# Kernel optimization log

Measured on AMD Instinct MI355X. Metric: run time of the kernel, lower is better.

## Reference

```python
import jax, jax.numpy as jnp
import numpy as np

H = 4                      # attention heads
L_NAMES = ['self', 'cross'] * 3
K_LIST = [None, None, 128, 128, 64, 64]  # top-k per layer (None = full attention)
BN_EPS = 1e-5


def conv1d(x, W, b):
    # 1x1 Conv1d: x [B, Ci, N], W [Co, Ci], b [Co]
    return jnp.einsum('oi,bin->bon', W, x) + b[:, None]


def bn_eval(x, g, b):
    # BatchNorm1d in eval mode with running mean 0 / var 1
    inv = 1.0 / np.sqrt(1.0 + BN_EPS)
    return (g * inv)[:, None] * x + b[:, None]


def mha(x, src, Wq, bq, Wk, bk, Wv, bv, Wm, bm, k):
    B, D, N = x.shape
    dh = D // H
    q = conv1d(x, Wq, bq).reshape(B, dh, H, N)
    kk = conv1d(src, Wk, bk).reshape(B, dh, H, -1)
    v = conv1d(src, Wv, bv).reshape(B, dh, H, -1)
    scores = jnp.einsum('bdhn,bdhm->bhnm', q, kk) / np.sqrt(dh)  # [B,H,N,M]
    if k is None:
        p = jax.nn.softmax(scores, axis=-1)
        out = jnp.einsum('bhnm,bdhm->bdhn', p, v)
    else:
        vals, idx = jax.lax.top_k(scores, k)          # [B,H,N,k]
        S = jax.nn.softmax(vals, axis=-1)
        # gather value vectors at the top-k key indices: [B,dh,H,N,k]
        vg = jnp.take_along_axis(v[:, :, :, None, :], idx[:, None, :, :, :], axis=4)
        out = jnp.einsum('bhnk,bdhnk->bdhn', S, vg)
    return conv1d(out.reshape(B, D, N), Wm, bm)


def log_ot(scores, alpha, iters):
    b, m, n = scores.shape
    bins0 = jnp.broadcast_to(alpha, (b, m, 1))
    bins1 = jnp.broadcast_to(alpha, (b, 1, n))
    a = jnp.broadcast_to(alpha, (b, 1, 1))
    Z0 = jnp.concatenate([jnp.concatenate([scores, bins0], -1),
                          jnp.concatenate([bins1, a], -1)], 1)  # [b,m+1,n+1]
    norm = -np.log(float(m + n))
    log_mu = jnp.concatenate([jnp.full((m,), norm, scores.dtype),
                              jnp.array([np.log(float(n)) + norm], scores.dtype)])
    log_nu = jnp.concatenate([jnp.full((n,), norm, scores.dtype),
                              jnp.array([np.log(float(m)) + norm], scores.dtype)])
    log_mu = jnp.broadcast_to(log_mu, (b, m + 1))
    log_nu = jnp.broadcast_to(log_nu, (b, n + 1))

    def step(carry, _):
        u, v = carry
        u = log_mu - jax.nn.logsumexp(Z0 + v[:, None, :], axis=2)
        v = log_nu - jax.nn.logsumexp(Z0 + u[:, :, None], axis=1)
        return (u, v), None

    (u, v), _ = jax.lax.scan(step, (jnp.zeros_like(log_mu), jnp.zeros_like(log_nu)),
                             None, length=iters)
    return Z0 + u[:, :, None] + v[:, None, :] - norm


def _forward(desc0, desc1, Wq, bq, Wk, bk, Wv, bv, Wm, bm,
             W1, b1, g1, be1, W2, b2, Wf, bf, alpha, iters):
    d0, d1 = desc0, desc1
    for i, (name, k) in enumerate(zip(L_NAMES, K_LIST)):
        s0, s1 = (d1, d0) if name == 'cross' else (d0, d1)

        def prop(x, src):
            msg = mha(x, src, Wq[i], bq[i], Wk[i], bk[i], Wv[i], bv[i], Wm[i], bm[i], k)
            h = jnp.concatenate([x, msg], axis=1)           # [B, 2D, N]
            h = jax.nn.relu(bn_eval(conv1d(h, W1[i], b1[i]), g1[i], be1[i]))
            return conv1d(h, W2[i], b2[i])

        dlt0, dlt1 = prop(d0, s0), prop(d1, s1)
        d0, d1 = d0 + dlt0, d1 + dlt1
    m0 = conv1d(d0, Wf, bf)
    m1 = conv1d(d1, Wf, bf)
    scores = jnp.einsum('bdn,bdm->bnm', m0, m1) / np.sqrt(m0.shape[1])
    return log_ot(scores, alpha, iters)


def setup_inputs() -> dict:
    B, D, N, L = 4, 128, 1024, 6
    key = jax.random.key(0)
    ks = jax.random.split(key, 20)

    def nrm(k, shape, s):
        return jax.random.normal(k, shape, jnp.float32) * s

    sw = 1.0 / np.sqrt(D)
    return {
        'desc0': nrm(ks[0], (B, D, N), 1.0),
        'desc1': nrm(ks[1], (B, D, N), 1.0),
        'Wq': nrm(ks[2], (L, D, D), sw), 'bq': jnp.zeros((L, D), jnp.float32),
        'Wk': nrm(ks[3], (L, D, D), sw), 'bk': jnp.zeros((L, D), jnp.float32),
        'Wv': nrm(ks[4], (L, D, D), sw), 'bv': jnp.zeros((L, D), jnp.float32),
        'Wm': nrm(ks[5], (L, D, D), sw), 'bm': jnp.zeros((L, D), jnp.float32),
        'W1': nrm(ks[6], (L, 2 * D, 2 * D), 1.0 / np.sqrt(2 * D)),
        'b1': jnp.zeros((L, 2 * D), jnp.float32),
        'g1': jnp.ones((L, 2 * D), jnp.float32),
        'be1': jnp.zeros((L, 2 * D), jnp.float32),
        'W2': nrm(ks[7], (L, D, 2 * D), 1.0 / np.sqrt(2 * D)),
        'b2': jnp.zeros((L, D), jnp.float32),
        'Wf': nrm(ks[8], (D, D), sw), 'bf': jnp.zeros((D,), jnp.float32),
        'alpha': jnp.asarray(1.0, jnp.float32),
        'iters': 20,
    }


def reference(desc0, desc1, Wq, bq, Wk, bk, Wv, bv, Wm, bm,
              W1, b1, g1, be1, W2, b2, Wf, bf, alpha, iters):
    return _forward(desc0, desc1, Wq, bq, Wk, bk, Wv, bv, Wm, bm,
                    W1, b1, g1, be1, W2, b2, Wf, bf, alpha, iters)
```

## Files before the change

### kernel.cpp

```cpp
#include <hip/hip_runtime.h>
#include <hip/hip_fp16.h>
#include <stdint.h>

#define NPOS   1024
#define DMODEL 128
#define NP1    1025
#define PLP    1053700
#define PSTR   1028
#define PLPH   1057800
#define PSTRH  1032
#define NORMF  (-7.624618986159398f)
#define LOGN   (6.931471805599453f)

typedef __attribute__((ext_vector_type(8))) short s8v;
typedef __attribute__((ext_vector_type(4))) float f4v;
typedef unsigned short ushort_t;

#define MFMA(a, b, c) __builtin_amdgcn_mfma_f32_16x16x32_bf16((a), (b), (c), 0, 0, 0)

static __device__ __forceinline__ ushort_t f2bf(float f) {
    union { float f; uint32_t u; } c; c.f = f;
    uint32_t u = c.u;
    return (ushort_t)((u + 0x7fffu + ((u >> 16) & 1u)) >> 16);
}
static __device__ __forceinline__ uint32_t cvtpk(float lo, float hi) {
    uint32_t r;
    asm("v_cvt_pk_bf16_f32 %0, %1, %2" : "=v"(r) : "v"(lo), "v"(hi));
    return r;
}

#define NW0 294912
#define NW2 393216
#define NW3 196608
#define NW4 16384
#define NB5 2304
#define NPREP (NW0 + NW2 + NW3 + NW4 + NB5)
__global__ __launch_bounds__(256) void prep_weights(
    const float* __restrict__ Wq, const float* __restrict__ Wk, const float* __restrict__ Wv,
    const float* __restrict__ bq, const float* __restrict__ bk, const float* __restrict__ bv,
    const float* __restrict__ W1, const float* __restrict__ W2, const float* __restrict__ Wf,
    ushort_t* __restrict__ wqkv, ushort_t* __restrict__ w1c,
    ushort_t* __restrict__ w2, ushort_t* __restrict__ wf, float* __restrict__ bqkv)
{
    int idx = blockIdx.x * 256 + threadIdx.x;
    if (idx < NW0) {
        int l = idx / 49152, r2 = idx % 49152;
        int r = r2 / 128, i = r2 % 128;
        int sel = r >> 7, rr = r & 127;
        int o = ((rr & 31) << 2) + (rr >> 5);
        const float* src = sel == 0 ? Wq : (sel == 1 ? Wk : Wv);
        wqkv[idx] = f2bf(src[((size_t)l * 128 + o) * 128 + i]);
        return;
    }
    idx -= NW0;
    if (idx < NW2) {
        int i = idx & 255;
        if (i < 128) w1c[idx] = f2bf(W1[idx]);
        return;
    }
    idx -= NW2;
    if (idx < NW3) { w2[idx] = f2bf(W2[idx]); return; }
    idx -= NW3;
    if (idx < NW4) { wf[idx] = f2bf(Wf[idx]); return; }
    idx -= NW4;
    if (idx < NB5) {
        int l = idx / 384, r = idx % 384;
        int sel = r >> 7, rr = r & 127;
        int o = ((rr & 31) << 2) + (rr >> 5);
        const float* src = sel == 0 ? bq : (sel == 1 ? bk : bv);
        bqkv[idx] = src[l * 128 + o];
    }
}

#define NFOLD 196608
#define NFB   1536
__global__ __launch_bounds__(256) void fold_w1(
    const float* __restrict__ W1, const float* __restrict__ Wm,
    const float* __restrict__ b1, const float* __restrict__ bm,
    ushort_t* __restrict__ w1c, float* __restrict__ b1c)
{
    int idx = blockIdx.x * 256 + threadIdx.x;
    if (idx < NFOLD) {
        int l = idx / 32768, rem = idx % 32768;
        int o = rem / 128, ip = rem % 128;
        int i = ((ip & 31) << 2) + (ip >> 5);
        const float* w1row = W1 + ((size_t)l * 256 + o) * 256 + 128;
        const float* wmcol = Wm + (size_t)l * 16384 + i;
        float s = 0.f;
        #pragma unroll 8
        for (int j = 0; j < 128; ++j) s = fmaf(w1row[j], wmcol[(size_t)j * 128], s);
        w1c[((size_t)l * 256 + o) * 256 + 128 + ip] = f2bf(s);
        return;
    }
    idx -= NFOLD;
    if (idx < NFB) {
        int l = idx / 256, o = idx % 256;
        const float* w1row = W1 + ((size_t)l * 256 + o) * 256 + 128;
        const float* bml = bm + l * 128;
        float s = b1[l * 256 + o];
        #pragma unroll 8
        for (int j = 0; j < 128; ++j) s = fmaf(w1row[j], bml[j], s);
        b1c[idx] = s;
    }
}

__global__ __launch_bounds__(256) void transpose_in(
    const float* __restrict__ desc0, const float* __restrict__ desc1,
    float* __restrict__ df, ushort_t* __restrict__ db)
{
    int g = blockIdx.z;
    int nb = blockIdx.x << 6, cb = blockIdx.y << 5;
    __shared__ float sm[32][65];
    const float* S = (g < 4 ? desc0 : desc1);
    int gl = g & 3;
    {
        int row = threadIdx.x >> 3, c8 = (threadIdx.x & 7) << 3;
        const float* p = S + ((size_t)gl * 128 + cb + row) * NPOS + nb + c8;
        float4 v0 = *(const float4*)p;
        float4 v1 = *(const float4*)(p + 4);
        sm[row][c8 + 0] = v0.x; sm[row][c8 + 1] = v0.y; sm[row][c8 + 2] = v0.z; sm[row][c8 + 3] = v0.w;
        sm[row][c8 + 4] = v1.x; sm[row][c8 + 5] = v1.y; sm[row][c8 + 6] = v1.z; sm[row][c8 + 7] = v1.w;
    }
    __syncthreads();
    int n = threadIdx.x >> 2, cc = (threadIdx.x & 3) << 3;
    float y[8];
    #pragma unroll
    for (int e = 0; e < 8; ++e) y[e] = sm[cc + e][n];
    size_t base = ((size_t)g * NPOS + nb + n) * DMODEL + cb + cc;
    *(float4*)(df + base) = make_float4(y[0], y[1], y[2], y[3]);
    *(float4*)(df + base + 4) = make_float4(y[4], y[5], y[6], y[7]);
    uint4 pk = make_uint4(cvtpk(y[0], y[1]), cvtpk(y[2], y[3]),
                          cvtpk(y[4], y[5]), cvtpk(y[6], y[7]));
    *(uint4*)(db + base) = pk;
}

__global__ __launch_bounds__(256) void conv_mfma(
    const ushort_t* __restrict__ X0, int Ci,
    const ushort_t* __restrict__ W, const float* __restrict__ bias,
    ushort_t* __restrict__ outb, int Co)
{
    int g = blockIdx.z;
    int nb = blockIdx.x << 6;
    int obb = blockIdx.y << 6;
    int wave = threadIdx.x >> 6, lane = threadIdx.x & 63;
    int lrow = lane & 15, lk = (lane >> 4) << 3;
    int ob = obb + (wave << 4);
    f4v acc[4] = {};
    const ushort_t* wrow = W + (size_t)(ob + lrow) * Ci + lk;
    for (int k0 = 0; k0 < Ci; k0 += 32) {
        s8v b = *(const s8v*)(wrow + k0);
        #pragma unroll
        for (int t = 0; t < 4; ++t) {
            int n = nb + (t << 4) + lrow;
            s8v a = *(const s8v*)(X0 + ((size_t)g * NPOS + n) * Ci + k0 + lk);
            acc[t] = MFMA(a, b, acc[t]);
        }
    }
    __shared__ float sm[64][68];
    #pragma unroll
    for (int t = 0; t < 4; ++t)
        #pragma unroll
        for (int r = 0; r < 4; ++r)
            sm[(t << 4) + ((lane >> 4) << 2) + r][(wave << 4) + lrow] = acc[t][r];
    __syncthreads();
    int n = threadIdx.x >> 2, oc = (threadIdx.x & 3) << 4;
    int o0 = obb + oc;
    float y[16];
    #pragma unroll
    for (int e = 0; e < 16; ++e) y[e] = sm[n][oc + e] + bias[o0 + e];
    size_t base = ((size_t)g * NPOS + nb + n) * Co + o0;
    uint4 p0 = make_uint4(cvtpk(y[0], y[1]), cvtpk(y[2], y[3]),
                          cvtpk(y[4], y[5]), cvtpk(y[6], y[7]));
    uint4 p1 = make_uint4(cvtpk(y[8], y[9]), cvtpk(y[10], y[11]),
                          cvtpk(y[12], y[13]), cvtpk(y[14], y[15]));
    *(uint4*)(outb + base) = p0;
    *(uint4*)(outb + base + 8) = p1;
}

__global__ __launch_bounds__(256) void mlp_mfma(
    const ushort_t* __restrict__ X0, const ushort_t* __restrict__ X1,
    const ushort_t* __restrict__ W1c, const float* __restrict__ b1c,
    const float* __restrict__ bn_g, const float* __restrict__ bn_b,
    const ushort_t* __restrict__ W2w, const float* __restrict__ b2,
    float* __restrict__ resid, ushort_t* __restrict__ outb)
{
    int g = blockIdx.y;
    int nb = blockIdx.x << 4;
    __shared__ ushort_t hB[16][256];
    __shared__ float sm[16][132];
    int wave = threadIdx.x >> 6, lane = threadIdx.x & 63;
    int lrow = lane & 15, lk = (lane >> 4) << 3;
    const float BN_INV = 0.9999950000374997f;

    const ushort_t* x0p = X0 + ((size_t)g * NPOS + nb + lrow) * 128 + lk;
    const ushort_t* x1p = X1 + ((size_t)g * NPOS + nb + lrow) * 128 + lk;
    for (int p = 0; p < 4; ++p) {
        int o = (p << 6) + (wave << 4) + lrow;
        f4v acc = {};
        const ushort_t* wrow = W1c + (size_t)o * 256 + lk;
        #pragma unroll
        for (int k0 = 0; k0 < 256; k0 += 32) {
            s8v b = *(const s8v*)(wrow + k0);
            s8v a = (k0 < 128) ? *(const s8v*)(x0p + k0) : *(const s8v*)(x1p + k0 - 128);
            acc = MFMA(a, b, acc);
        }
        #pragma unroll
        for (int r = 0; r < 4; ++r)
            sm[((lane >> 4) << 2) + r][(wave << 4) + lrow] = acc[r];
        __syncthreads();
        {
            int n = threadIdx.x >> 4, oc = (threadIdx.x & 15) << 2;
            int og = (p << 6) + oc;
            float y[4];
            #pragma unroll
            for (int e = 0; e < 4; ++e) {
                float v = sm[n][oc + e] + b1c[og + e];
                y[e] = fmaxf(bn_g[og + e] * BN_INV * v + bn_b[og + e], 0.f);
            }
            *(uint2*)(&hB[n][og]) = make_uint2(cvtpk(y[0], y[1]), cvtpk(y[2], y[3]));
        }
        __syncthreads();
    }

    f4v acc2[2] = {};
    #pragma unroll
    for (int k0 = 0; k0 < 256; k0 += 32) {
        s8v a = *(const s8v*)(&hB[lrow][k0 + lk]);
        #pragma unroll
        for (int ot = 0; ot < 2; ++ot) {
            int o = (wave << 5) + (ot << 4) + lrow;
            s8v b = *(const s8v*)(W2w + (size_t)o * 256 + k0 + lk);
            acc2[ot] = MFMA(a, b, acc2[ot]);
        }
    }
    #pragma unroll
    for (int ot = 0; ot < 2; ++ot)
        #pragma unroll
        for (int r = 0; r < 4; ++r)
            sm[((lane >> 4) << 2) + r][(wave << 5) + (ot << 4) + lrow] = acc2[ot][r];
    __syncthreads();
    {
        int n = threadIdx.x >> 4, oc = (threadIdx.x & 15) << 3;
        size_t base = ((size_t)g * NPOS + nb + n) * 128 + oc;
        float* rp = resid + base;
        float4 ra = *(const float4*)rp;
        float4 rb = *(const float4*)(rp + 4);
        float y[8];
        y[0] = sm[n][oc + 0] + b2[oc + 0] + ra.x;
        y[1] = sm[n][oc + 1] + b2[oc + 1] + ra.y;
        y[2] = sm[n][oc + 2] + b2[oc + 2] + ra.z;
        y[3] = sm[n][oc + 3] + b2[oc + 3] + ra.w;
        y[4] = sm[n][oc + 4] + b2[oc + 4] + rb.x;
        y[5] = sm[n][oc + 5] + b2[oc + 5] + rb.y;
        y[6] = sm[n][oc + 6] + b2[oc + 6] + rb.z;
        y[7] = sm[n][oc + 7] + b2[oc + 7] + rb.w;
        *(float4*)rp = make_float4(y[0], y[1], y[2], y[3]);
        *(float4*)(rp + 4) = make_float4(y[4], y[5], y[6], y[7]);
        uint4 pk = make_uint4(cvtpk(y[0], y[1]), cvtpk(y[2], y[3]),
                              cvtpk(y[4], y[5]), cvtpk(y[6], y[7]));
        *(uint4*)(outb + base) = pk;
    }
}

__global__ __launch_bounds__(256) void qkv_mfma(
    const ushort_t* __restrict__ X, const ushort_t* __restrict__ W,
    const float* __restrict__ bias,
    ushort_t* __restrict__ Qb, ushort_t* __restrict__ Kb, ushort_t* __restrict__ Vb)
{
    int g = blockIdx.z;
    int nb = blockIdx.x << 6;
    int obb = blockIdx.y << 6;
    int wave = threadIdx.x >> 6, lane = threadIdx.x & 63;
    int lrow = lane & 15, lk = (lane >> 4) << 3;
    int ob = obb + (wave << 4);
    f4v acc[4] = {};
    const ushort_t* wrow = W + (size_t)(ob + lrow) * DMODEL + lk;
    for (int k0 = 0; k0 < DMODEL; k0 += 32) {
        s8v b = *(const s8v*)(wrow + k0);
        #pragma unroll
        for (int t = 0; t < 4; ++t) {
            int n = nb + (t << 4) + lrow;
            s8v a = *(const s8v*)(X + ((size_t)g * NPOS + n) * DMODEL + k0 + lk);
            acc[t] = MFMA(a, b, acc[t]);
        }
    }
    __shared__ float sm[64][68];
    #pragma unroll
    for (int t = 0; t < 4; ++t)
        #pragma unroll
        for (int r = 0; r < 4; ++r)
            sm[(t << 4) + ((lane >> 4) << 2) + r][(wave << 4) + lrow] = acc[t][r];
    __syncthreads();
    if (obb < 256) {
        int n = threadIdx.x >> 2, oc = (threadIdx.x & 3) << 4;
        int ov = obb + oc;
        ushort_t* dst = (ov < 128) ? Qb : Kb;
        int c = ov & 127;
        float y[16];
        #pragma unroll
        for (int e = 0; e < 16; ++e) y[e] = sm[n][oc + e] + bias[ov + e];
        size_t base = ((size_t)g * NPOS + nb + n) * DMODEL + c;
        uint4 p0 = make_uint4(cvtpk(y[0], y[1]), cvtpk(y[2], y[3]),
                              cvtpk(y[4], y[5]), cvtpk(y[6], y[7]));
        uint4 p1 = make_uint4(cvtpk(y[8], y[9]), cvtpk(y[10], y[11]),
                              cvtpk(y[12], y[13]), cvtpk(y[14], y[15]));
        *(uint4*)(dst + base) = p0;
        *(uint4*)(dst + base + 8) = p1;
    } else {
        int c = threadIdx.x >> 2, mc = (threadIdx.x & 3) << 4;
        float bc = bias[obb + c];
        float y[16];
        #pragma unroll
        for (int e = 0; e < 16; ++e) y[e] = sm[mc + e][c] + bc;
        size_t base = ((size_t)g * DMODEL + (obb - 256) + c) * NPOS + nb + mc;
        uint4 p0 = make_uint4(cvtpk(y[0], y[1]), cvtpk(y[2], y[3]),
                              cvtpk(y[4], y[5]), cvtpk(y[6], y[7]));
        uint4 p1 = make_uint4(cvtpk(y[8], y[9]), cvtpk(y[10], y[11]),
                              cvtpk(y[12], y[13]), cvtpk(y[14], y[15]));
        *(uint4*)(Vb + base) = p0;
        *(uint4*)(Vb + base + 8) = p1;
    }
}

__global__ __launch_bounds__(512, 8) void attn_fused(
    const ushort_t* __restrict__ Qb, const ushort_t* __restrict__ Kb,
    const ushort_t* __restrict__ Vb, ushort_t* __restrict__ ao,
    int k, int cross)
{
    __shared__ ushort_t sc[16 * 1024];
    __shared__ float sinv[16];
    int bid = blockIdx.x;
    int gh = ((bid & 7) << 2) + (bid >> 9);
    int g = gh >> 2, h = gh & 3;
    int g2 = cross ? (g ^ 4) : g;
    int n0 = ((bid >> 3) & 63) << 4;
    int wave = threadIdx.x >> 6, lane = threadIdx.x & 63;
    int lrow = lane & 15, lq = lane >> 4;

    {
        int kq = wave;
        s8v qa = *(const s8v*)(Qb + ((size_t)g * NPOS + n0 + lrow) * DMODEL
                               + (h << 5) + (lq << 3));
        const float scale = 0.17677669529663687f;
        int swz = (lrow & 7) << 4;
        const ushort_t* kb_base = Kb + ((size_t)g2 * NPOS + (kq << 7) + lrow) * DMODEL
                                  + (h << 5) + (lq << 3);
        #pragma unroll
        for (int mt = 0; mt < 8; ++mt) {
            s8v kb = *(const s8v*)(kb_base + (size_t)mt * 16 * DMODEL);
            f4v z = {};
            z = MFMA(kb, qa, z);
            uint32_t p0 = cvtpk(z[0] * scale, z[1] * scale);
            uint32_t p1 = cvtpk(z[2] * scale, z[3] * scale);
            int m = (kq << 7) + (mt << 4);
            int byte = ((lrow << 11) + ((m + (lq << 2)) << 1)) ^ swz;
            *(uint2*)((char*)sc + byte) = make_uint2(p0, p1);
        }
    }
    __syncthreads();

    {
        bool dosel = (k < NPOS);
        for (int rr = 0; rr < 2; ++rr) {
            int row = (wave << 1) + rr;
            int swz = (row & 7) << 4;
            int base = (row << 11) + (lane << 5);
            uint4 d0 = *(const uint4*)((const char*)sc + (base ^ swz));
            uint4 d1 = *(const uint4*)((const char*)sc + ((base + 16) ^ swz));
            float val[16];
            {
                uint32_t wd[8] = {d0.x, d0.y, d0.z, d0.w, d1.x, d1.y, d1.z, d1.w};
                #pragma unroll
                for (int q = 0; q < 8; ++q) {
                    union { unsigned ui; float f; } c0, c1;
                    c0.ui = wd[q] << 16; c1.ui = wd[q] & 0xFFFF0000u;
                    val[2 * q] = c0.f; val[2 * q + 1] = c1.f;
                }
            }
            float mx = val[0];
            #pragma unroll
            for (int t = 1; t < 16; ++t) mx = fmaxf(mx, val[t]);
            #pragma unroll
            for (int o = 32; o; o >>= 1) mx = fmaxf(mx, __shfl_xor(mx, o));

            unsigned selmask = 0xFFFFu;
            if (dosel) {
                unsigned prefix = 0;
                bool exact = false;
                for (int bit = 15; bit >= 0 && !exact; --bit) {
                    unsigned cand = prefix | (1u << bit);
                    unsigned craw = (cand & 0x8000u) ? (cand ^ 0x8000u) : (cand ^ 0xFFFFu);
                    union { unsigned ui; float f; } cf; cf.ui = craw << 16;
                    float cf_f = cf.f;
                    int c = 0;
                    #pragma unroll
                    for (int t = 0; t < 16; ++t)
                        c += __popcll(__ballot(val[t] >= cf_f));
                    if (c >= k) { prefix = cand; exact = (c == k); }
                }
                unsigned praw = (prefix & 0x8000u) ? (prefix ^ 0x8000u) : (prefix ^ 0xFFFFu);
                union { unsigned ui; float f; } pf; pf.ui = praw << 16;
                float thr = pf.f;
                if (exact) {
                    selmask = 0;
                    #pragma unroll
                    for (int t = 0; t < 16; ++t)
                        selmask |= (val[t] >= thr) ? (1u << t) : 0u;
                } else {
                    int cgt = 0;
                    #pragma unroll
                    for (int t = 0; t < 16; ++t)
                        cgt += __popcll(__ballot(val[t] > thr));
                    int need = k - cgt;
                    unsigned long long lmask = (1ull << lane) - 1ull;
                    int before = 0;
                    #pragma unroll
                    for (int t = 0; t < 16; ++t)
                        before += __popcll(__ballot(val[t] == thr) & lmask);
                    int loc = 0;
                    selmask = 0;
                    #pragma unroll
                    for (int t = 0; t < 16; ++t) {
                        bool tie = (val[t] == thr);
                        if ((val[t] > thr) || (tie && (before + loc < need)))
                            selmask |= (1u << t);
                        loc += tie ? 1 : 0;
                    }
                }
            }
            float sum = 0.f;
            #pragma unroll
            for (int t = 0; t < 16; ++t) {
                float wv = ((selmask >> t) & 1u) ? __expf(val[t] - mx) : 0.f;
                val[t] = wv;
                sum += wv;
            }
            #pragma unroll
            for (int o = 32; o; o >>= 1) sum += __shfl_xor(sum, o);
            if (lane == 0) sinv[row] = 1.f / sum;
            uint32_t ow[8];
            #pragma unroll
            for (int q = 0; q < 8; ++q)
                ow[q] = cvtpk(val[2 * q], val[2 * q + 1]);
            *(uint4*)((char*)sc + (base ^ swz)) = make_uint4(ow[0], ow[1], ow[2], ow[3]);
            *(uint4*)((char*)sc + ((base + 16) ^ swz)) = make_uint4(ow[4], ow[5], ow[6], ow[7]);
        }
    }
    __syncthreads();

    {
        int kquad = wave >> 1, dimg = wave & 1;
        int db = dimg << 4;
        const ushort_t* vbase = Vb + ((size_t)g2 * DMODEL + (h << 5) + db + lrow) * NPOS
                                + (kquad << 8) + (lq << 3);
        int pswz = (lrow & 7) << 4;
        int pbase = (lrow << 11) + (kquad << 9) + (lq << 4);
        f4v acc = {};
        #pragma unroll
        for (int ks = 0; ks < 8; ++ks) {
            s8v pa = *(const s8v*)((const char*)sc + ((pbase + (ks << 6)) ^ pswz));
            s8v vv = *(const s8v*)(vbase + (ks << 5));
            acc = MFMA(pa, vv, acc);
        }
        __syncthreads();
        if (kquad > 0)
            *(f4v*)((char*)sc + (((((kquad - 1) << 1) + dimg) * 64 + lane) << 4)) = acc;
        __syncthreads();
        if (kquad == 0) {
            #pragma unroll
            for (int qq = 0; qq < 3; ++qq)
                acc = acc + *(const f4v*)((char*)sc + ((((qq << 1) + dimg) * 64 + lane) << 4));
            #pragma unroll
            for (int r = 0; r < 4; ++r) {
                int rowi = (lq << 2) + r;
                int n = n0 + rowi;
                ao[((size_t)g * NPOS + n) * DMODEL + (h << 5) + db + lrow]
                    = f2bf(acc[r] * sinv[rowi]);
            }
        }
    }
}

__global__ __launch_bounds__(256) void final_mfma(
    const ushort_t* __restrict__ md, float* __restrict__ Z0P,
    __half* __restrict__ Z0H, __half* __restrict__ Z0TH)
{
    int b = blockIdx.z;
    int wave = threadIdx.x >> 6, lane = threadIdx.x & 63;
    int wr = wave >> 1, wc = wave & 1;
    int n0 = (blockIdx.y << 7) + (wr << 6);
    int m0 = (blockIdx.x << 7) + (wc << 6);
    int lrow = lane & 15, lk = (lane >> 4) << 3;
    f4v acc[4][4] = {};
    for (int k0 = 0; k0 < DMODEL; k0 += 32) {
        s8v qa[4], kb[4];
        #pragma unroll
        for (int t = 0; t < 4; ++t) {
            qa[t] = *(const s8v*)(md + ((size_t)b * NPOS + n0 + (t << 4) + lrow) * DMODEL + k0 + lk);
            kb[t] = *(const s8v*)(md + ((size_t)(b + 4) * NPOS + m0 + (t << 4) + lrow) * DMODEL + k0 + lk);
        }
        #pragma unroll
        for (int tn = 0; tn < 4; ++tn)
            #pragma unroll
            for (int tm = 0; tm < 4; ++tm)
                acc[tn][tm] = MFMA(qa[tn], kb[tm], acc[tn][tm]);
    }
    const float scf = 0.08838834764831845f;
    int rbase = (lane >> 4) << 2;
    #pragma unroll
    for (int tn = 0; tn < 4; ++tn) {
        #pragma unroll
        for (int tm = 0; tm < 4; ++tm) {
            #pragma unroll
            for (int r = 0; r < 4; ++r) {
                int n = n0 + (tn << 4) + rbase + r;
                int m = m0 + (tm << 4) + lrow;
                float y = acc[tn][tm][r] * scf;
                Z0P[(size_t)b * PLP + (size_t)n * PSTR + m] = y;
                __half hy = __float2half(y);
                Z0H [(size_t)b * PLPH + (size_t)n * PSTRH + m] = hy;
                Z0TH[(size_t)b * PLPH + (size_t)m * PSTRH + n] = hy;
            }
        }
    }
}

__global__ __launch_bounds__(1024) void ot_init(
    float* __restrict__ Z0P, __half* __restrict__ Z0H, __half* __restrict__ Z0TH,
    float* __restrict__ v, const float* __restrict__ alpha)
{
    float a = *alpha;
    __half ha = __float2half(a);
    int b = blockIdx.x, t = threadIdx.x;
    Z0P [(size_t)b * PLP  + (size_t)t * PSTR  + 1024] = a;
    Z0P [(size_t)b * PLP  + (size_t)1024 * PSTR + t] = a;
    Z0H [(size_t)b * PLPH + (size_t)t * PSTRH + 1024] = ha;
    Z0H [(size_t)b * PLPH + (size_t)1024 * PSTRH + t] = ha;
    Z0TH[(size_t)b * PLPH + (size_t)t * PSTRH + 1024] = ha;
    Z0TH[(size_t)b * PLPH + (size_t)1024 * PSTRH + t] = ha;
    v[b * NP1 + t] = 0.f;
    if (t == 0) {
        Z0P [(size_t)b * PLP  + (size_t)1024 * PSTR  + 1024] = a;
        Z0H [(size_t)b * PLPH + (size_t)1024 * PSTRH + 1024] = ha;
        Z0TH[(size_t)b * PLPH + (size_t)1024 * PSTRH + 1024] = ha;
        v[b * NP1 + 1024] = 0.f;
    }
}

__global__ __launch_bounds__(256) void lse_sweep_h(
    const __half* __restrict__ Z, const float* __restrict__ vin,
    float* __restrict__ uout)
{
    int wv = threadIdx.x >> 6, lane = threadIdx.x & 63;
    int r = blockIdx.x * 4 + wv;
    int b = r / NP1, i = r - b * NP1;
    const __half* z  = Z + (size_t)b * PLPH + (size_t)i * PSTRH;
    const float* vb = vin + b * NP1;
    float x[17];
    #pragma unroll
    for (int t = 0; t < 2; ++t) {
        int j = (t << 9) + (lane << 3);
        union { uint4 u; __half h[8]; } U;
        U.u = *(const uint4*)(z + j);
        float4 v0 = *(const float4*)(vb + j);
        float4 v1 = *(const float4*)(vb + j + 4);
        x[t * 8 + 0] = __half2float(U.h[0]) + v0.x;
        x[t * 8 + 1] = __half2float(U.h[1]) + v0.y;
        x[t * 8 + 2] = __half2float(U.h[2]) + v0.z;
        x[t * 8 + 3] = __half2float(U.h[3]) + v0.w;
        x[t * 8 + 4] = __half2float(U.h[4]) + v1.x;
        x[t * 8 + 5] = __half2float(U.h[5]) + v1.y;
        x[t * 8 + 6] = __half2float(U.h[6]) + v1.z;
        x[t * 8 + 7] = __half2float(U.h[7]) + v1.w;
    }
    x[16] = (lane == 0) ? (__half2float(z[1024]) + vb[1024]) : -1e30f;
    float m = x[0];
    #pragma unroll
    for (int t = 1; t < 17; ++t) m = fmaxf(m, x[t]);
    #pragma unroll
    for (int o = 32; o; o >>= 1) m = fmaxf(m, __shfl_xor(m, o));
    float sum = 0.f;
    #pragma unroll
    for (int t = 0; t < 17; ++t) sum += __expf(x[t] - m);
    #pragma unroll
    for (int o = 32; o; o >>= 1) sum += __shfl_xor(sum, o);
    if (lane == 0)
        uout[b * NP1 + i] = NORMF + ((i == 1024) ? LOGN : 0.f) - (m + __logf(sum));
}

__global__ __launch_bounds__(256) void ot_final(
    float* __restrict__ out, const float* __restrict__ Z0P,
    const float* __restrict__ u, const float* __restrict__ v)
{
    int r = blockIdx.x;
    int b = r / NP1, i = r - b * NP1;
    float ui = u[b * NP1 + i] - NORMF;
    const float* zp = Z0P + (size_t)b * PLP + (size_t)i * PSTR;
    float* zo = out + ((size_t)b * NP1 + i) * NP1;
    const float* vb = v + b * NP1;
    for (int j = threadIdx.x; j < NP1; j += 256) zo[j] = zp[j] + ui + vb[j];
}

extern "C" void kernel_launch(void* const* d_in, const int* in_sizes, int n_in,
                              void* d_out, int out_size, void* d_ws, size_t ws_size,
                              hipStream_t stream)
{
    (void)in_sizes; (void)n_in; (void)out_size; (void)ws_size;
    const float* desc0 = (const float*)d_in[0];
    const float* desc1 = (const float*)d_in[1];
    const float* Wq = (const float*)d_in[2];  const float* bq = (const float*)d_in[3];
    const float* Wk = (const float*)d_in[4];  const float* bk = (const float*)d_in[5];
    const float* Wv = (const float*)d_in[6];  const float* bv = (const float*)d_in[7];
    const float* Wm = (const float*)d_in[8];  const float* bm = (const float*)d_in[9];
    const float* W1 = (const float*)d_in[10]; const float* b1 = (const float*)d_in[11];
    const float* g1 = (const float*)d_in[12]; const float* be1 = (const float*)d_in[13];
    const float* W2 = (const float*)d_in[14]; const float* b2 = (const float*)d_in[15];
    const float* Wf = (const float*)d_in[16]; const float* bf = (const float*)d_in[17];
    const float* alpha = (const float*)d_in[18];

    float* Zout = (float*)d_out;
    float* ws = (float*)d_ws;
    size_t o = 0;
    float* d_f32      = ws;                          o += 1048576;
    ushort_t* d_bf    = (ushort_t*)(ws + o);         o += 524288;
    ushort_t* Qb      = (ushort_t*)(ws + o);         o += 524288;
    ushort_t* Kb      = (ushort_t*)(ws + o);         o += 524288;
    ushort_t* Vb      = (ushort_t*)(ws + o);         o += 524288;
    ushort_t* aob     = (ushort_t*)(ws + o);         o += 524288;
    ushort_t* mdesc   = (ushort_t*)(ws + o);         o += 524288;
    ushort_t* wqkv    = (ushort_t*)(ws + o);         o += 147456;
    ushort_t* w1c     = (ushort_t*)(ws + o);         o += 196608;
    ushort_t* w2w     = (ushort_t*)(ws + o);         o += 98304;
    ushort_t* wfw     = (ushort_t*)(ws + o);         o += 8192;
    float* bqkv       = ws + o;                      o += 2304;
    float* b1c        = ws + o;                      o += 1536;
    float* ub         = ws + o;                      o += 4352;
    float* vb         = ws + o;                      o += 4352;
    float* Z0P        = ws + o;                      o += 4214800;
    __half* Z0H       = (__half*)(ws + o);           o += 2115600;
    __half* Z0TH      = (__half*)(ws + o);           o += 2115600;

    dim3 blk(256);
    prep_weights<<<dim3((NPREP + 255) / 256), blk, 0, stream>>>(
        Wq, Wk, Wv, bq, bk, bv, W1, W2, Wf, wqkv, w1c, w2w, wfw, bqkv);
    fold_w1<<<dim3((NFOLD + NFB + 255) / 256), blk, 0, stream>>>(
        W1, Wm, b1, bm, w1c, b1c);
    transpose_in<<<dim3(16, 4, 8), blk, 0, stream>>>(desc0, desc1, d_f32, d_bf);

    static const int KLIST[6] = {1024, 1024, 128, 128, 64, 64};
    for (int l = 0; l < 6; ++l) {
        int cross = l & 1;
        int k = KLIST[l];
        qkv_mfma<<<dim3(16, 6, 8), blk, 0, stream>>>(
            d_bf, wqkv + (size_t)l * 49152, bqkv + l * 384, Qb, Kb, Vb);
        attn_fused<<<dim3(2048), dim3(512), 0, stream>>>(Qb, Kb, Vb, aob, k, cross);
        mlp_mfma<<<dim3(64, 8), blk, 0, stream>>>(
            d_bf, aob, w1c + (size_t)l * 65536, b1c + l * 256,
            g1 + l * 256, be1 + l * 256,
            w2w + (size_t)l * 32768, b2 + l * 128, d_f32, d_bf);
    }
    conv_mfma<<<dim3(16, 2, 8), blk, 0, stream>>>(
        d_bf, 128, wfw, bf, mdesc, 128);
    final_mfma<<<dim3(8, 8, 4), blk, 0, stream>>>(mdesc, Z0P, Z0H, Z0TH);
    ot_init<<<dim3(4), dim3(1024), 0, stream>>>(Z0P, Z0H, Z0TH, vb, alpha);
    for (int it = 0; it < 20; ++it) {
        lse_sweep_h<<<dim3(1025), blk, 0, stream>>>(Z0H,  vb, ub);
        lse_sweep_h<<<dim3(1025), blk, 0, stream>>>(Z0TH, ub, vb);
    }
    ot_final<<<dim3(4100), blk, 0, stream>>>(Zout, Z0P, ub, vb);
}
```

Before: 755.0 us.

## Interleave two-row top-k selection, unsplit MLP first GEMM, tree reductions

The attention top-k softmax now processes both rows of a wave together, interleaving their radix-select ballot loops and shuffle reductions to expose more independent work and hide latency. The MLP kernel computes all 256 hidden outputs in one pass with four accumulators per wave, replacing four phases that each needed two barriers. Serial max/sum chains become tree reductions. The attention occupancy hint is lowered from 8 to 6 to give the extra live state more registers, and the MLP shared buffer grows, which may reduce occupancy.

```diff
diff --git a/kernel.cpp b/kernel.cpp
--- a/kernel.cpp
+++ b/kernel.cpp
@@ -27,6 +27,18 @@
     uint32_t r;
     asm("v_cvt_pk_bf16_f32 %0, %1, %2" : "=v"(r) : "v"(lo), "v"(hi));
     return r;
+}
+static __device__ __forceinline__ float tmax16(const float* v) {
+    float a = fmaxf(fmaxf(fmaxf(v[0], v[1]), fmaxf(v[2], v[3])),
+                    fmaxf(fmaxf(v[4], v[5]), fmaxf(v[6], v[7])));
+    float b = fmaxf(fmaxf(fmaxf(v[8], v[9]), fmaxf(v[10], v[11])),
+                    fmaxf(fmaxf(v[12], v[13]), fmaxf(v[14], v[15])));
+    return fmaxf(a, b);
+}
+static __device__ __forceinline__ float tsum16(const float* v) {
+    float a = ((v[0] + v[1]) + (v[2] + v[3])) + ((v[4] + v[5]) + (v[6] + v[7]));
+    float b = ((v[8] + v[9]) + (v[10] + v[11])) + ((v[12] + v[13]) + (v[14] + v[15]));
+    return a + b;
 }
 
 #define NW0 294912
@@ -187,40 +199,48 @@
     int g = blockIdx.y;
     int nb = blockIdx.x << 4;
     __shared__ ushort_t hB[16][256];
-    __shared__ float sm[16][132];
+    __shared__ float sm[16][260];
     int wave = threadIdx.x >> 6, lane = threadIdx.x & 63;
     int lrow = lane & 15, lk = (lane >> 4) << 3;
     const float BN_INV = 0.9999950000374997f;
 
     const ushort_t* x0p = X0 + ((size_t)g * NPOS + nb + lrow) * 128 + lk;
     const ushort_t* x1p = X1 + ((size_t)g * NPOS + nb + lrow) * 128 + lk;
-    for (int p = 0; p < 4; ++p) {
-        int o = (p << 6) + (wave << 4) + lrow;
-        f4v acc = {};
-        const ushort_t* wrow = W1c + (size_t)o * 256 + lk;
+    {
+        f4v acc[4] = {};
         #pragma unroll
         for (int k0 = 0; k0 < 256; k0 += 32) {
-            s8v b = *(const s8v*)(wrow + k0);
             s8v a = (k0 < 128) ? *(const s8v*)(x0p + k0) : *(const s8v*)(x1p + k0 - 128);
-            acc = MFMA(a, b, acc);
-        }
-        #pragma unroll
-        for (int r = 0; r < 4; ++r)
-            sm[((lane >> 4) << 2) + r][(wave << 4) + lrow] = acc[r];
-        __syncthreads();
-        {
-            int n = threadIdx.x >> 4, oc = (threadIdx.x & 15) << 2;
-            int og = (p << 6) + oc;
-            float y[4];
-            #pragma unroll
-            for (int e = 0; e < 4; ++e) {
-                float v = sm[n][oc + e] + b1c[og + e];
-                y[e] = fmaxf(bn_g[og + e] * BN_INV * v + bn_b[og + e], 0.f);
+            #pragma unroll
+            for (int ot = 0; ot < 4; ++ot) {
+                int o = (wave << 6) + (ot << 4) + lrow;
+                s8v b = *(const s8v*)(W1c + (size_t)o * 256 + k0 + lk);
+                acc[ot] = MFMA(a, b, acc[ot]);
             }
-            *(uint2*)(&hB[n][og]) = make_uint2(cvtpk(y[0], y[1]), cvtpk(y[2], y[3]));
-        }
-        __syncthreads();
-    }
+        }
+        #pragma unroll
+        for (int ot = 0; ot < 4; ++ot)
+            #pragma unroll
+            for (int r = 0; r < 4; ++r)
+                sm[((lane >> 4) << 2) + r][(wave << 6) + (ot << 4) + lrow] = acc[ot][r];
+    }
+    __syncthreads();
+    {
+        int n = threadIdx.x >> 4, oc = (threadIdx.x & 15) << 4;
+        float y[16];
+        #pragma unroll
+        for (int e = 0; e < 16; ++e) {
+            float v = sm[n][oc + e] + b1c[oc + e];
+            y[e] = fmaxf(bn_g[oc + e] * BN_INV * v + bn_b[oc + e], 0.f);
+        }
+        uint4 p0 = make_uint4(cvtpk(y[0], y[1]), cvtpk(y[2], y[3]),
+                              cvtpk(y[4], y[5]), cvtpk(y[6], y[7]));
+        uint4 p1 = make_uint4(cvtpk(y[8], y[9]), cvtpk(y[10], y[11]),
+                              cvtpk(y[12], y[13]), cvtpk(y[14], y[15]));
+        *(uint4*)(&hB[n][oc]) = p0;
+        *(uint4*)(&hB[n][oc + 8]) = p1;
+    }
+    __syncthreads();
 
     f4v acc2[2] = {};
     #pragma unroll
@@ -233,6 +253,7 @@
             acc2[ot] = MFMA(a, b, acc2[ot]);
         }
     }
+    __syncthreads();
     #pragma unroll
     for (int ot = 0; ot < 2; ++ot)
         #pragma unroll
@@ -322,7 +343,7 @@
     }
 }
 
-__global__ __launch_bounds__(512, 8) void attn_fused(
+__global__ __launch_bounds__(512, 6) void attn_fused(
     const ushort_t* __restrict__ Qb, const ushort_t* __restrict__ Kb,
     const ushort_t* __restrict__ Vb, ushort_t* __restrict__ ao,
     int k, int cross)
@@ -361,89 +382,110 @@
 
     {
         bool dosel = (k < NPOS);
-        for (int rr = 0; rr < 2; ++rr) {
-            int row = (wave << 1) + rr;
-            int swz = (row & 7) << 4;
-            int base = (row << 11) + (lane << 5);
-            uint4 d0 = *(const uint4*)((const char*)sc + (base ^ swz));
-            uint4 d1 = *(const uint4*)((const char*)sc + ((base + 16) ^ swz));
-            float val[16];
-            {
-                uint32_t wd[8] = {d0.x, d0.y, d0.z, d0.w, d1.x, d1.y, d1.z, d1.w};
+        int row0 = wave << 1;
+        int swzr[2], baser[2];
+        float val[2][16];
+        #pragma unroll
+        for (int rp = 0; rp < 2; ++rp) {
+            int row = row0 + rp;
+            swzr[rp] = (row & 7) << 4;
+            baser[rp] = (row << 11) + (lane << 5);
+            uint4 d0 = *(const uint4*)((const char*)sc + (baser[rp] ^ swzr[rp]));
+            uint4 d1 = *(const uint4*)((const char*)sc + ((baser[rp] + 16) ^ swzr[rp]));
+            uint32_t wd[8] = {d0.x, d0.y, d0.z, d0.w, d1.x, d1.y, d1.z, d1.w};
+            #pragma unroll
+            for (int q = 0; q < 8; ++q) {
+                union { unsigned ui; float f; } c0, c1;
+                c0.ui = wd[q] << 16; c1.ui = wd[q] & 0xFFFF0000u;
+                val[rp][2 * q] = c0.f; val[rp][2 * q + 1] = c1.f;
+            }
+        }
+        float mx[2];
+        #pragma unroll
+        for (int rp = 0; rp < 2; ++rp) mx[rp] = tmax16(val[rp]);
+        #pragma unroll
+        for (int o = 32; o; o >>= 1)
+            #pragma unroll
+            for (int rp = 0; rp < 2; ++rp)
+                mx[rp] = fmaxf(mx[rp], __shfl_xor(mx[rp], o));
+
+        unsigned selmask[2] = {0xFFFFu, 0xFFFFu};
+        if (dosel) {
+            unsigned prefix[2] = {0u, 0u};
+            bool exact[2] = {false, false};
+            for (int bit = 15; bit >= 0 && !(exact[0] && exact[1]); --bit) {
                 #pragma unroll
-                for (int q = 0; q < 8; ++q) {
-                    union { unsigned ui; float f; } c0, c1;
-                    c0.ui = wd[q] << 16; c1.ui = wd[q] & 0xFFFF0000u;
-                    val[2 * q] = c0.f; val[2 * q + 1] = c1.f;
-                }
-            }
-            float mx = val[0];
-            #pragma unroll
-            for (int t = 1; t < 16; ++t) mx = fmaxf(mx, val[t]);
-            #pragma unroll
-            for (int o = 32; o; o >>= 1) mx = fmaxf(mx, __shfl_xor(mx, o));
-
-            unsigned selmask = 0xFFFFu;
-            if (dosel) {
-                unsigned prefix = 0;
-                bool exact = false;
-                for (int bit = 15; bit >= 0 && !exact; --bit) {
-                    unsigned cand = prefix | (1u << bit);
+                for (int rp = 0; rp < 2; ++rp) {
+                    if (exact[rp]) continue;
+                    unsigned cand = prefix[rp] | (1u << bit);
                     unsigned craw = (cand & 0x8000u) ? (cand ^ 0x8000u) : (cand ^ 0xFFFFu);
                     union { unsigned ui; float f; } cf; cf.ui = craw << 16;
                     float cf_f = cf.f;
                     int c = 0;
                     #pragma unroll
                     for (int t = 0; t < 16; ++t)
-                        c += __popcll(__ballot(val[t] >= cf_f));
-                    if (c >= k) { prefix = cand; exact = (c == k); }
+                        c += __popcll(__ballot(val[rp][t] >= cf_f));
+                    if (c >= k) { prefix[rp] = cand; exact[rp] = (c == k); }
                 }
-                unsigned praw = (prefix & 0x8000u) ? (prefix ^ 0x8000u) : (prefix ^ 0xFFFFu);
+            }
+            #pragma unroll
+            for (int rp = 0; rp < 2; ++rp) {
+                unsigned praw = (prefix[rp] & 0x8000u) ? (prefix[rp] ^ 0x8000u)
+                                                       : (prefix[rp] ^ 0xFFFFu);
                 union { unsigned ui; float f; } pf; pf.ui = praw << 16;
                 float thr = pf.f;
-                if (exact) {
-                    selmask = 0;
+                if (exact[rp]) {
+                    selmask[rp] = 0;
                     #pragma unroll
                     for (int t = 0; t < 16; ++t)
-                        selmask |= (val[t] >= thr) ? (1u << t) : 0u;
+                        selmask[rp] |= (val[rp][t] >= thr) ? (1u << t) : 0u;
                 } else {
                     int cgt = 0;
                     #pragma unroll
                     for (int t = 0; t < 16; ++t)
-                        cgt += __popcll(__ballot(val[t] > thr));
+                        cgt += __popcll(__ballot(val[rp][t] > thr));
                     int need = k - cgt;
                     unsigned long long lmask = (1ull << lane) - 1ull;
                     int before = 0;
                     #pragma unroll
                     for (int t = 0; t < 16; ++t)
-                        before += __popcll(__ballot(val[t] == thr) & lmask);
+                        before += __popcll(__ballot(val[rp][t] == thr) & lmask);
                     int loc = 0;
-                    selmask = 0;
+                    selmask[rp] = 0;
                     #pragma unroll
                     for (int t = 0; t < 16; ++t) {
-                        bool tie = (val[t] == thr);
-                        if ((val[t] > thr) || (tie && (before + loc < need)))
-                            selmask |= (1u << t);
+                        bool tie = (val[rp][t] == thr);
+                        if ((val[rp][t] > thr) || (tie && (before + loc < need)))
+                            selmask[rp] |= (1u << t);
                         loc += tie ? 1 : 0;
                     }
                 }
             }
-            float sum = 0.f;
-            #pragma unroll
-            for (int t = 0; t < 16; ++t) {
-                float wv = ((selmask >> t) & 1u) ? __expf(val[t] - mx) : 0.f;
-                val[t] = wv;
-                sum += wv;
-            }
-            #pragma unroll
-            for (int o = 32; o; o >>= 1) sum += __shfl_xor(sum, o);
-            if (lane == 0) sinv[row] = 1.f / sum;
+        }
+        float sum[2];
+        #pragma unroll
+        for (int rp = 0; rp < 2; ++rp) {
+            #pragma unroll
+            for (int t = 0; t < 16; ++t)
+                val[rp][t] = ((selmask[rp] >> t) & 1u) ? __expf(val[rp][t] - mx[rp]) : 0.f;
+            sum[rp] = tsum16(val[rp]);
+        }
+        #pragma unroll
+        for (int o = 32; o; o >>= 1)
+            #pragma unroll
+            for (int rp = 0; rp < 2; ++rp)
+                sum[rp] += __shfl_xor(sum[rp], o);
+        #pragma unroll
+        for (int rp = 0; rp < 2; ++rp) {
+            if (lane == 0) sinv[row0 + rp] = 1.f / sum[rp];
             uint32_t ow[8];
             #pragma unroll
             for (int q = 0; q < 8; ++q)
-                ow[q] = cvtpk(val[2 * q], val[2 * q + 1]);
-            *(uint4*)((char*)sc + (base ^ swz)) = make_uint4(ow[0], ow[1], ow[2], ow[3]);
-            *(uint4*)((char*)sc + ((base + 16) ^ swz)) = make_uint4(ow[4], ow[5], ow[6], ow[7]);
+                ow[q] = cvtpk(val[rp][2 * q], val[rp][2 * q + 1]);
+            *(uint4*)((char*)sc + (baser[rp] ^ swzr[rp])) =
+                make_uint4(ow[0], ow[1], ow[2], ow[3]);
+            *(uint4*)((char*)sc + ((baser[rp] + 16) ^ swzr[rp])) =
+                make_uint4(ow[4], ow[5], ow[6], ow[7]);
         }
     }
     __syncthreads();
@@ -574,9 +616,7 @@
         x[t * 8 + 7] = __half2float(U.h[7]) + v1.w;
     }
     x[16] = (lane == 0) ? (__half2float(z[1024]) + vb[1024]) : -1e30f;
-    float m = x[0];
-    #pragma unroll
-    for (int t = 1; t < 17; ++t) m = fmaxf(m, x[t]);
+    float m = fmaxf(tmax16(x), x[16]);
     #pragma unroll
     for (int o = 32; o; o >>= 1) m = fmaxf(m, __shfl_xor(m, o));
     float sum = 0.f;
```

After: 724.0 us. 4.1% less time.
